# Performance work log

Measured on AMD Instinct MI355X. Metric: run time of the kernel, lower is better.

The kernel has to match this reference:

```python
import jax, jax.numpy as jnp
import numpy as np

EPS = 1.1920929e-07  # torch RMSNorm default eps = finfo(fp32).eps


def _rmsnorm(x, w):
    return x * jax.lax.rsqrt(jnp.mean(x * x, axis=-1, keepdims=True) + EPS) * w


def setup_inputs() -> dict:
    B, S, D, H, SD = 2, 2048, 1024, 16, 64
    ks = jax.random.split(jax.random.key(0), 16)
    scale = 0.02
    return {
        "x": jax.random.normal(ks[0], (B, S, D), jnp.float32),
        "gamma": jax.random.normal(ks[1], (1, 1, D), jnp.float32),
        "beta": jax.random.normal(ks[2], (1, 1, D), jnp.float32),
        "state": jax.random.normal(ks[3], (B, SD), jnp.float32),
        # weights stored as (in, out) so y = x @ W
        "w_qkv": jax.random.normal(ks[4], (D, 3 * D), jnp.float32) * scale,
        "w_o": jax.random.normal(ks[5], (D, D), jnp.float32) * scale,
        "w_gate": jax.random.normal(ks[6], (D, 3 * D), jnp.float32) * scale,
        "w_up": jax.random.normal(ks[7], (D, 3 * D), jnp.float32) * scale,
        "w_down": jax.random.normal(ks[8], (3 * D, D), jnp.float32) * scale,
        "norm1_w": jnp.ones((D,), jnp.float32),
        "norm2_w": jnp.ones((D,), jnp.float32),
        "w_state_mod": jax.random.normal(ks[9], (SD, 2 * D), jnp.float32) * scale,
        "w_h2s": jax.random.normal(ks[10], (D, SD), jnp.float32) * scale,
        "w_sgate": jax.random.normal(ks[11], (2 * SD, SD), jnp.float32) * scale,
    }


def reference(x, gamma, beta, state, w_qkv, w_o, w_gate, w_up, w_down,
              norm1_w, norm2_w, w_state_mod, w_h2s, w_sgate):
    B, S, D = x.shape
    H = 16
    hd = D // H

    # state-conditioned FiLM modulation
    state_mod = state @ w_state_mod                      # (B, 2D)
    state_gamma = 1.0 + state_mod[:, :D][:, None, :]     # (B, 1, D)
    state_beta = state_mod[:, D:][:, None, :]
    full_gamma = gamma * state_gamma
    full_beta = beta + state_beta

    # attention branch
    h = _rmsnorm(x, norm1_w) * full_gamma + full_beta
    qkv = (h @ w_qkv).reshape(B, S, 3, H, hd)
    q = qkv[:, :, 0].transpose(0, 2, 1, 3)               # (B, H, S, hd)
    k = qkv[:, :, 1].transpose(0, 2, 1, 3)
    v = qkv[:, :, 2].transpose(0, 2, 1, 3)
    scores = jnp.einsum('bhqd,bhkd->bhqk', q, k) / np.sqrt(hd).astype(np.float32)
    causal = jnp.tril(jnp.ones((S, S), bool))
    scores = jnp.where(causal, scores, -jnp.inf)
    attn = jax.nn.softmax(scores, axis=-1)
    out = jnp.einsum('bhqk,bhkd->bhqd', attn, v).transpose(0, 2, 1, 3).reshape(B, S, D)
    x = x + out @ w_o

    # SwiGLU FFN branch (same FiLM params)
    h2 = _rmsnorm(x, norm2_w) * full_gamma + full_beta
    gate = jax.nn.silu(h2 @ w_gate)
    x = x + (gate * (h2 @ w_up)) @ w_down

    # recurrent state update
    new_info = jnp.mean(x, axis=1) @ w_h2s               # (B, SD)
    update_gate = jax.nn.sigmoid(jnp.concatenate([state, new_info], axis=-1) @ w_sgate)
    new_state = state * (1.0 - update_gate) + new_info * update_gate
    return x, new_state
```

## Files before the change

kernel.cpp:

```cpp
#include <hip/hip_runtime.h>
#include <hip/hip_bf16.h>

#define EPS_RMS 1.1920929e-07f

constexpr int B_ = 2, S_ = 2048, D_ = 1024, H_ = 16, HD_ = 64, SD_ = 64;
constexpr int M_ = B_ * S_;
constexpr int D3_ = 3 * D_;

using short8 = __attribute__((ext_vector_type(8))) short;
using f32x4  = __attribute__((ext_vector_type(4))) float;
using f32x16 = __attribute__((ext_vector_type(16))) float;
typedef int v2i __attribute__((ext_vector_type(2)));

static __device__ __forceinline__ ushort f2bf(float x) {
  __hip_bfloat16 h = __float2bfloat16(x);
  return *reinterpret_cast<ushort*>(&h);
}
static __device__ __forceinline__ float bf2f(ushort u) {
  __hip_bfloat16 h;
  *reinterpret_cast<ushort*>(&h) = u;
  return __bfloat162float(h);
}
static __device__ __forceinline__ unsigned pk2(float lo, float hi) {
  return (unsigned)f2bf(lo) | ((unsigned)f2bf(hi) << 16);
}
static __device__ __forceinline__ v2i swap32(int a, int b) {
  return __builtin_amdgcn_permlane32_swap(a, b, false, false);
}
struct alignas(8) bf4 { ushort a, b, c, d; };

static __device__ __forceinline__ void gload16(const ushort* g, ushort* l) {
  __builtin_amdgcn_global_load_lds(
      (const __attribute__((address_space(1))) unsigned int*)g,
      (__attribute__((address_space(3))) unsigned int*)l, 16, 0, 0);
}

__global__ void film_kernel(const float* __restrict__ state,
                            const float* __restrict__ w_sm,
                            const float* __restrict__ gamma,
                            const float* __restrict__ beta,
                            float* __restrict__ fg, float* __restrict__ fb) {
  int c = blockIdx.x * 256 + threadIdx.x;
  int b = blockIdx.y;
  float acc = 0.f;
#pragma unroll 8
  for (int k = 0; k < SD_; ++k)
    acc += state[b * SD_ + k] * w_sm[k * (2 * D_) + c];
  if (c < D_) fg[b * D_ + c] = gamma[c] * (1.f + acc);
  else        fb[b * D_ + (c - D_)] = beta[c - D_] + acc;
}

__global__ __launch_bounds__(256) void rmsnorm_film_kernel(
    const float* __restrict__ X, const float* __restrict__ nw,
    const float* __restrict__ fg, const float* __restrict__ fb,
    ushort* __restrict__ Hout) {
  int row = blockIdx.x;
  int b = row / S_;
  int t = threadIdx.x;
  const float4* x4 = (const float4*)(X + (size_t)row * D_);
  float4 xv = x4[t];
  float ss = xv.x * xv.x + xv.y * xv.y + xv.z * xv.z + xv.w * xv.w;
#pragma unroll
  for (int off = 32; off >= 1; off >>= 1) ss += __shfl_xor(ss, off);
  __shared__ float red[4];
  if ((t & 63) == 0) red[t >> 6] = ss;
  __syncthreads();
  float tot = red[0] + red[1] + red[2] + red[3];
  float scale = rsqrtf(tot / (float)D_ + EPS_RMS);
  int d = t * 4;
  const float4 nw4 = *(const float4*)(nw + d);
  const float4 g4  = *(const float4*)(fg + b * D_ + d);
  const float4 b4  = *(const float4*)(fb + b * D_ + d);
  bf4 hv;
  hv.a = f2bf(xv.x * scale * nw4.x * g4.x + b4.x);
  hv.b = f2bf(xv.y * scale * nw4.y * g4.y + b4.y);
  hv.c = f2bf(xv.z * scale * nw4.z * g4.z + b4.z);
  hv.d = f2bf(xv.w * scale * nw4.w * g4.w + b4.w);
  *(bf4*)(Hout + (size_t)row * D_ + d) = hv;
}

__global__ __launch_bounds__(256) void transpose_bf16(
    const float* __restrict__ W, ushort* __restrict__ Wt, int K, int N) {
  __shared__ float tile[32][33];
  int n0 = blockIdx.x * 32, k0 = blockIdx.y * 32;
  int t = threadIdx.x;
  int c = t & 31, r = t >> 5;
#pragma unroll
  for (int p = 0; p < 4; ++p)
    tile[r + 8 * p][c] = W[(size_t)(k0 + r + 8 * p) * N + n0 + c];
  __syncthreads();
#pragma unroll
  for (int p = 0; p < 4; ++p)
    Wt[(size_t)(n0 + r + 8 * p) * K + k0 + c] = f2bf(tile[c][r + 8 * p]);
}

__global__ __launch_bounds__(256) void transpose_bf16_dual(
    const float* __restrict__ W0, ushort* __restrict__ T0,
    const float* __restrict__ W1, ushort* __restrict__ T1, int K, int N) {
  const float* W = blockIdx.z ? W1 : W0;
  ushort* Wt = blockIdx.z ? T1 : T0;
  __shared__ float tile[32][33];
  int n0 = blockIdx.x * 32, k0 = blockIdx.y * 32;
  int t = threadIdx.x;
  int c = t & 31, r = t >> 5;
#pragma unroll
  for (int p = 0; p < 4; ++p)
    tile[r + 8 * p][c] = W[(size_t)(k0 + r + 8 * p) * N + n0 + c];
  __syncthreads();
#pragma unroll
  for (int p = 0; p < 4; ++p)
    Wt[(size_t)(n0 + r + 8 * p) * K + k0 + c] = f2bf(tile[c][r + 8 * p]);
}

static __device__ __forceinline__ void mfma_tile(
    const char* Au, const char* Bu, f32x4 (&acc)[4][4],
    int l15, int l4, int swz, int wr, int wc) {
#pragma unroll
  for (int kk = 0; kk < 2; ++kk) {
    int tslot = ((kk * 4 + l4) ^ swz) << 4;
    short8 a[4], b[4];
#pragma unroll
    for (int i = 0; i < 4; ++i) {
      int arow = wr * 64 + i * 16 + l15;
      int brow = wc * 64 + i * 16 + l15;
      a[i] = *(const short8*)(Au + arow * 128 + tslot);
      b[i] = *(const short8*)(Bu + brow * 128 + tslot);
    }
#pragma unroll
    for (int m = 0; m < 4; ++m)
#pragma unroll
      for (int n = 0; n < 4; ++n)
        acc[m][n] = __builtin_amdgcn_mfma_f32_16x16x32_bf16(a[m], b[n], acc[m][n], 0, 0, 0);
  }
}

static __device__ __forceinline__ void block_swizzle(int bid, int M, int N,
                                                     int& bm, int& bn) {
  int nbn = N >> 7;
  int nb  = nbn * (M >> 7);
  int qx  = nb >> 3;
  int lin = (bid & 7) * qx + (bid >> 3);
  int grp = lin / (nbn << 3), rem = lin % (nbn << 3);
  bm = ((grp << 3) + (rem & 7)) << 7;
  bn = (rem >> 3) << 7;
}

template<int EPI>
__global__ __launch_bounds__(256, 3) void gemm_mfma(
    const ushort* __restrict__ A, const ushort* __restrict__ Bt,
    const float* __restrict__ Res,
    float* __restrict__ Cf, ushort* __restrict__ Cb, ushort* __restrict__ VtP,
    int M, int N, int K) {
  __shared__ ushort smem[16384];
  char* Au = (char*)smem;
  char* Bu = (char*)(smem + 8192);
  int t = threadIdx.x;
  int bm, bn;
  block_swizzle(blockIdx.x, M, N, bm, bn);

  int lane = t & 63, wid = t >> 6;
  int wr = wid >> 1, wc = wid & 1;
  int l15 = lane & 15, l4 = lane >> 4;
  int swz = l15 & 7;

  const ushort* gA[4];
  const ushort* gB[4];
  ushort* lA[4];
  ushort* lB[4];
#pragma unroll
  for (int p = 0; p < 4; ++p) {
    int seg = p * 4 + wid;
    int flat = seg * 64 + lane;
    int row = flat >> 3, sl = flat & 7;
    int gc = ((sl ^ (row & 7)) << 3);
    gA[p] = A  + (size_t)(bm + row) * K + gc;
    gB[p] = Bt + (size_t)(bn + row) * K + gc;
    lA[p] = smem + seg * 512;
    lB[p] = smem + 8192 + seg * 512;
  }

  f32x4 acc[4][4];
#pragma unroll
  for (int m = 0; m < 4; ++m)
#pragma unroll
    for (int n = 0; n < 4; ++n) acc[m][n] = (f32x4){0.f, 0.f, 0.f, 0.f};

  int nk = K >> 6;
  for (int kt = 0; kt < nk; ++kt) {
    __syncthreads();
#pragma unroll
    for (int p = 0; p < 4; ++p) {
      gload16(gA[p], lA[p]);
      gload16(gB[p], lB[p]);
      gA[p] += 64; gB[p] += 64;
    }
    __syncthreads();
    mfma_tile(Au, Bu, acc, l15, l4, swz, wr, wc);
  }

  if constexpr (EPI == 3) {
#pragma unroll
    for (int m = 0; m < 4; ++m)
#pragma unroll
      for (int n = 0; n < 4; ++n) {
        int row0 = bm + wr * 64 + m * 16 + l4 * 4;
        int col  = bn + wc * 64 + n * 16 + l15;
#pragma unroll
        for (int j = 0; j < 4; ++j) {
          size_t idx = (size_t)(row0 + j) * (size_t)N + col;
          Cf[idx] = Res[idx] + acc[m][n][j];
        }
      }
  } else {
    __syncthreads();
    ushort* Es = smem;
    bool vblk = (bn >= 2048);
#pragma unroll
    for (int m = 0; m < 4; ++m)
#pragma unroll
      for (int n = 0; n < 4; ++n) {
        int rb0 = wr * 64 + m * 16 + l4 * 4;
        int c   = wc * 64 + n * 16 + l15;
#pragma unroll
        for (int j = 0; j < 4; ++j) {
          float v = acc[m][n][j];
          int r = rb0 + j;
          if (vblk) Es[c * 128 + (r ^ ((c & 15) << 3))] = f2bf(v);
          else      Es[r * 128 + c] = f2bf(v);
        }
      }
    __syncthreads();
    if (vblk) {
#pragma unroll
      for (int p = 0; p < 8; ++p) {
        int flat = p * 256 + t;
        int c = flat >> 4, r8 = (flat & 15) * 8;
        int vc = bn - 2048 + c, hh = vc >> 6, dd = vc & 63;
        int bbv = bm >> 11, s0 = (bm & 2047) + r8;
        *(short8*)(VtP + ((((size_t)bbv * 16 + hh) * 64 + dd) << 11) + s0) =
            *(const short8*)&Es[c * 128 + (r8 ^ ((c & 15) << 3))];
      }
    } else {
#pragma unroll
      for (int p = 0; p < 8; ++p) {
        int flat = p * 256 + t;
        int r = flat >> 4, c8 = (flat & 15) * 8;
        *(short8*)(Cb + (size_t)(bm + r) * N + bn + c8) = *(const short8*)&Es[r * 128 + c8];
      }
    }
  }
}

__global__ __launch_bounds__(256, 2) void gemm_dual(
    const ushort* __restrict__ A, const ushort* __restrict__ Gt,
    const ushort* __restrict__ Ut, ushort* __restrict__ Cb,
    int M, int N, int K) {
  __shared__ ushort smem[24576];
  char* Au = (char*)smem;
  char* Gu = (char*)(smem + 8192);
  char* Uu = (char*)(smem + 16384);
  int t = threadIdx.x;
  int bm, bn;
  block_swizzle(blockIdx.x, M, N, bm, bn);

  int lane = t & 63, wid = t >> 6;
  int wr = wid >> 1, wc = wid & 1;
  int l15 = lane & 15, l4 = lane >> 4;
  int swz = l15 & 7;

  const ushort* gA[4]; const ushort* gG[4]; const ushort* gU[4];
  ushort* lA[4]; ushort* lG[4]; ushort* lU[4];
#pragma unroll
  for (int p = 0; p < 4; ++p) {
    int seg = p * 4 + wid;
    int flat = seg * 64 + lane;
    int row = flat >> 3, sl = flat & 7;
    int gc = ((sl ^ (row & 7)) << 3);
    gA[p] = A  + (size_t)(bm + row) * K + gc;
    gG[p] = Gt + (size_t)(bn + row) * K + gc;
    gU[p] = Ut + (size_t)(bn + row) * K + gc;
    lA[p] = smem + seg * 512;
    lG[p] = smem + 8192 + seg * 512;
    lU[p] = smem + 16384 + seg * 512;
  }

  f32x4 ag[4][4], au[4][4];
#pragma unroll
  for (int m = 0; m < 4; ++m)
#pragma unroll
    for (int n = 0; n < 4; ++n) {
      ag[m][n] = (f32x4){0.f, 0.f, 0.f, 0.f};
      au[m][n] = (f32x4){0.f, 0.f, 0.f, 0.f};
    }

  int nk = K >> 6;
  for (int kt = 0; kt < nk; ++kt) {
    __syncthreads();
#pragma unroll
    for (int p = 0; p < 4; ++p) {
      gload16(gA[p], lA[p]);
      gload16(gG[p], lG[p]);
      gload16(gU[p], lU[p]);
      gA[p] += 64; gG[p] += 64; gU[p] += 64;
    }
    __syncthreads();
#pragma unroll
    for (int kk = 0; kk < 2; ++kk) {
      int tslot = ((kk * 4 + l4) ^ swz) << 4;
      short8 a[4], bg[4], bu[4];
#pragma unroll
      for (int i = 0; i < 4; ++i) {
        int arow = wr * 64 + i * 16 + l15;
        int brow = wc * 64 + i * 16 + l15;
        a[i]  = *(const short8*)(Au + arow * 128 + tslot);
        bg[i] = *(const short8*)(Gu + brow * 128 + tslot);
        bu[i] = *(const short8*)(Uu + brow * 128 + tslot);
      }
#pragma unroll
      for (int m = 0; m < 4; ++m)
#pragma unroll
        for (int n = 0; n < 4; ++n) {
          ag[m][n] = __builtin_amdgcn_mfma_f32_16x16x32_bf16(a[m], bg[n], ag[m][n], 0, 0, 0);
          au[m][n] = __builtin_amdgcn_mfma_f32_16x16x32_bf16(a[m], bu[n], au[m][n], 0, 0, 0);
        }
    }
  }

  __syncthreads();
  ushort* Es = smem;
#pragma unroll
  for (int m = 0; m < 4; ++m)
#pragma unroll
    for (int n = 0; n < 4; ++n) {
      int rb0 = wr * 64 + m * 16 + l4 * 4;
      int c   = wc * 64 + n * 16 + l15;
#pragma unroll
      for (int j = 0; j < 4; ++j) {
        float gv = ag[m][n][j];
        float v = gv / (1.f + __expf(-gv)) * au[m][n][j];
        Es[(rb0 + j) * 128 + c] = f2bf(v);
      }
    }
  __syncthreads();
#pragma unroll
  for (int p = 0; p < 8; ++p) {
    int flat = p * 256 + t;
    int r = flat >> 4, c8 = (flat & 15) * 8;
    *(short8*)(Cb + (size_t)(bm + r) * N + bn + c8) = *(const short8*)&Es[r * 128 + c8];
  }
}

__global__ __launch_bounds__(512, 2) void attn_mfma_kernel(
    const ushort* __restrict__ qkv,
    const ushort* __restrict__ Vt,
    ushort* __restrict__ AO) {
  __shared__ ushort lds[16384];
  const float SL2 = 0.125f * 1.44269504f;
  int t = threadIdx.x;
  int x = blockIdx.x;
  int lin = ((x & 7) << 5) + (x >> 3);
  int pp = lin & 7;
  int hb = lin >> 3;
  int h = hb & 15, bb = hb >> 4;
  int lane = t & 63, wv = t >> 6;
  int qi = wv >> 2, wsub = wv & 3;
  int qt = qi ? (15 - pp) : pp;
  int q0 = qt * 128;
  int l31 = lane & 31, g = lane >> 5;

  int qrow = q0 + wsub * 32 + l31;
  const ushort* qrow_ptr = qkv + (size_t)(bb * S_ + qrow) * 3072 + h * 64;
  short8 qf[4];
#pragma unroll
  for (int s = 0; s < 4; ++s) qf[s] = *(const short8*)(qrow_ptr + s * 16 + g * 8);

  f32x16 accO[2];
#pragma unroll
  for (int u = 0; u < 2; ++u)
#pragma unroll
    for (int r = 0; r < 16; ++r) accO[u][r] = 0.f;
  float m = -INFINITY, l = 0.f;
  int qg = qrow;
  int qmin = q0 + wsub * 32, qmax = qmin + 31;
  int nt = 2 * (16 - pp);

  const ushort* kbase = qkv + (size_t)(bb * S_) * 3072 + 1024 + h * 64;
  const ushort* vbase = Vt + ((size_t)(bb * 16 + h) * 64) * 2048;

  int srow = t >> 3, sslot = t & 7;
  int soff = srow * 64 + ((sslot ^ (srow & 7)) << 3);
  const ushort* kg0 = kbase + (size_t)srow * 3072 + sslot * 8;
  const ushort* vg0 = vbase + (size_t)srow * 2048 + sslot * 8;

  *(short8*)&lds[soff] = *(const short8*)kg0;
  *(short8*)&lds[4096 + soff] = *(const short8*)vg0;
  __syncthreads();

  for (int kti = 0; kti < nt; ++kti) {
    int cur = kti & 1;
    int kt = kti << 6;
    bool pf = (kti + 1 < nt);
    short8 rk, rv;
    if (pf) {
      rk = *(const short8*)(kg0 + (size_t)(kti + 1) * (64 * 3072));
      rv = *(const short8*)(vg0 + (kti + 1) * 64);
    }
    if (kt <= qmax) {
      const ushort* Kb = lds + cur * 8192;
      const ushort* Vb = Kb + 4096;

      f32x16 accT[2];
#pragma unroll
      for (int t2 = 0; t2 < 2; ++t2)
#pragma unroll
        for (int r = 0; r < 16; ++r) accT[t2][r] = 0.f;
      __builtin_amdgcn_s_setprio(1);
#pragma unroll
      for (int t2 = 0; t2 < 2; ++t2) {
        int key = 32 * t2 + l31;
#pragma unroll
        for (int s = 0; s < 4; ++s) {
          short8 kf = *(const short8*)&Kb[key * 64 + (((2 * s + g) ^ (key & 7)) << 3)];
          accT[t2] = __builtin_amdgcn_mfma_f32_32x32x16_bf16(kf, qf[s], accT[t2], 0, 0, 0);
        }
      }
      __builtin_amdgcn_s_setprio(0);

      bool need_mask = (kt + 63 > qmin);
      float p_[2][16];
      float pmax = -INFINITY;
#pragma unroll
      for (int t2 = 0; t2 < 2; ++t2)
#pragma unroll
        for (int r = 0; r < 16; ++r) {
          float v = accT[t2][r] * SL2;
          if (need_mask) {
            int key = kt + 32 * t2 + (r & 3) + 8 * (r >> 2) + 4 * g;
            if (key > qg) v = -INFINITY;
          }
          p_[t2][r] = v;
          pmax = fmaxf(pmax, v);
        }
      {
        v2i pm = swap32(__float_as_int(pmax), __float_as_int(pmax));
        pmax = fmaxf(pmax, __int_as_float(g ? pm.x : pm.y));
      }

      if (__any(pmax > m + 11.5f)) {
        float mnew = fmaxf(m, pmax);
        float corr = exp2f(m - mnew);
        m = mnew;
        l *= corr;
        float cr[16];
#pragma unroll
        for (int r = 0; r < 16; ++r) cr[r] = __shfl(corr, (r & 3) + 8 * (r >> 2) + 4 * g);
#pragma unroll
        for (int r = 0; r < 16; ++r) { accO[0][r] *= cr[r]; accO[1][r] *= cr[r]; }
      }
      float psum = 0.f;
#pragma unroll
      for (int t2 = 0; t2 < 2; ++t2)
#pragma unroll
        for (int r = 0; r < 16; ++r) {
          float e = exp2f(p_[t2][r] - m);
          p_[t2][r] = e;
          psum += e;
        }
      {
        v2i ps = swap32(__float_as_int(psum), __float_as_int(psum));
        psum += __int_as_float(g ? ps.x : ps.y);
      }
      l += psum;

#pragma unroll
      for (int s = 0; s < 4; ++s) {
        int ca = 2 * s, cb2 = 2 * s + 1;
        int ta = ca >> 2, ra = (ca & 3) * 4;
        int tb = cb2 >> 2, rbq = (cb2 & 3) * 4;
        int w0a = (int)pk2(p_[ta][ra], p_[ta][ra + 1]);
        int w1a = (int)pk2(p_[ta][ra + 2], p_[ta][ra + 3]);
        int w0b = (int)pk2(p_[tb][rbq], p_[tb][rbq + 1]);
        int w1b = (int)pk2(p_[tb][rbq + 2], p_[tb][rbq + 3]);
        v2i r0 = swap32(w0a, w0b);
        v2i r1 = swap32(w1a, w1b);
        union { int u[4]; short8 s8; } pa;
        pa.u[0] = r0.x;
        pa.u[1] = r1.x;
        pa.u[2] = r0.y;
        pa.u[3] = r1.y;
        __builtin_amdgcn_s_setprio(1);
#pragma unroll
        for (int u = 0; u < 2; ++u) {
          int d = 32 * u + l31;
          short8 vf = *(const short8*)&Vb[d * 64 + (((2 * s + g) ^ (d & 7)) << 3)];
          accO[u] = __builtin_amdgcn_mfma_f32_32x32x16_bf16(pa.s8, vf, accO[u], 0, 0, 0);
        }
        __builtin_amdgcn_s_setprio(0);
      }
    }
    if (pf) {
      ushort* dst = lds + (cur ^ 1) * 8192;
      *(short8*)&dst[soff] = rk;
      *(short8*)&dst[4096 + soff] = rv;
    }
    __syncthreads();
  }

  float linv = 1.f / l;
  float lr[16];
#pragma unroll
  for (int r = 0; r < 16; ++r) lr[r] = __shfl(linv, (r & 3) + 8 * (r >> 2) + 4 * g);
#pragma unroll
  for (int r = 0; r < 16; ++r) {
    int row = wv * 32 + (r & 3) + 8 * (r >> 2) + 4 * g;
    lds[row * 64 + l31]      = f2bf(accO[0][r] * lr[r]);
    lds[row * 64 + 32 + l31] = f2bf(accO[1][r] * lr[r]);
  }
  __syncthreads();
#pragma unroll
  for (int p = 0; p < 4; ++p) {
    int flat = p * 512 + t;
    int row = flat >> 3, slot = flat & 7;
    int qto = (row < 128) ? pp : (15 - pp);
    int grow = row & 127;
    *(short8*)(AO + (size_t)(bb * S_ + qto * 128 + grow) * 1024 + h * 64 + slot * 8) =
        *(const short8*)&lds[row * 64 + slot * 8];
  }
}

__global__ void colmean1(const float* __restrict__ X, float* __restrict__ part) {
  int d = blockIdx.x * 256 + threadIdx.x;
  int b = blockIdx.y;
  int ch = blockIdx.z;
  float s = 0.f;
  int s0 = ch * (S_ / 16);
  for (int i = 0; i < S_ / 16; ++i)
    s += X[(size_t)(b * S_ + s0 + i) * D_ + d];
  part[(b * 16 + ch) * D_ + d] = s;
}

__global__ __launch_bounds__(1024) void colmean2_state_kernel(
    const float* __restrict__ part, const float* __restrict__ state,
    const float* __restrict__ w_h2s, const float* __restrict__ w_sg,
    float* __restrict__ out_tail) {
  __shared__ float cms[2048];
  __shared__ float nis[128];
  int t = threadIdx.x;
#pragma unroll
  for (int i = 0; i < 2; ++i) {
    int idx = i * 1024 + t;
    int b = idx >> 10, d = idx & 1023;
    float s = 0.f;
#pragma unroll
    for (int c = 0; c < 16; ++c) s += part[(b * 16 + c) * D_ + d];
    cms[idx] = s * (1.f / (float)S_);
  }
  __syncthreads();
  {
    int out = t >> 3, ks = t & 7;
    int b = out >> 6, j = out & 63;
    float ni = 0.f;
    int k0 = ks * 128;
#pragma unroll 8
    for (int k = k0; k < k0 + 128; ++k)
      ni += cms[b * 1024 + k] * w_h2s[k * SD_ + j];
    ni += __shfl_xor(ni, 1);
    ni += __shfl_xor(ni, 2);
    ni += __shfl_xor(ni, 4);
    if (ks == 0) nis[out] = ni;
  }
  __syncthreads();
  if (t < 128) {
    int b = t >> 6, j = t & 63;
    float nv = nis[t];
    float g = 0.f;
#pragma unroll
    for (int k = 0; k < SD_; ++k) g += state[b * SD_ + k] * w_sg[k * SD_ + j];
#pragma unroll
    for (int k = 0; k < SD_; ++k) g += nis[b * SD_ + k] * w_sg[(SD_ + k) * SD_ + j];
    g = 1.f / (1.f + __expf(-g));
    float st = state[b * SD_ + j];
    out_tail[t] = st * (1.f - g) + nv * g;
  }
}

extern "C" void kernel_launch(void* const* d_in, const int* in_sizes, int n_in,
                              void* d_out, int out_size, void* d_ws, size_t ws_size,
                              hipStream_t stream) {
  const float* x      = (const float*)d_in[0];
  const float* gamma  = (const float*)d_in[1];
  const float* beta   = (const float*)d_in[2];
  const float* state  = (const float*)d_in[3];
  const float* w_qkv  = (const float*)d_in[4];
  const float* w_o    = (const float*)d_in[5];
  const float* w_gate = (const float*)d_in[6];
  const float* w_up   = (const float*)d_in[7];
  const float* w_down = (const float*)d_in[8];
  const float* norm1w = (const float*)d_in[9];
  const float* norm2w = (const float*)d_in[10];
  const float* w_sm   = (const float*)d_in[11];
  const float* w_h2s  = (const float*)d_in[12];
  const float* w_sg   = (const float*)d_in[13];
  float* out = (float*)d_out;

  float* ws = (float*)d_ws;
  float*  fg     = ws;
  float*  fb     = ws + 2048;
  float*  part   = ws + 8192;
  ushort* h_bf   = (ushort*)(ws + 65536);
  ushort* AO_bf  = (ushort*)(ws + 65536 + 2097152);
  ushort* wT     = (ushort*)(ws + 65536 + 2 * 2097152);
  ushort* wT2    = (ushort*)(ws + 65536 + 2 * 2097152 + 1572864);
  ushort* qkv_bf = (ushort*)(ws + 65536 + 2 * 2097152 + 2 * 1572864);
  ushort* Vt_g   = (ushort*)(ws + 65536 + 2 * 2097152 + 2 * 1572864 + 6291456);
  ushort* gu_bf  = qkv_bf;

  film_kernel<<<dim3(8, B_), 256, 0, stream>>>(state, w_sm, gamma, beta, fg, fb);
  rmsnorm_film_kernel<<<M_, 256, 0, stream>>>(x, norm1w, fg, fb, h_bf);
  transpose_bf16<<<dim3(D3_ / 32, D_ / 32), 256, 0, stream>>>(w_qkv, wT, D_, D3_);
  gemm_mfma<4><<<(D3_ / 128) * (M_ / 128), 256, 0, stream>>>(
      h_bf, wT, nullptr, nullptr, qkv_bf, Vt_g, M_, D3_, D_);
  attn_mfma_kernel<<<256, 512, 0, stream>>>(qkv_bf, Vt_g, AO_bf);
  transpose_bf16<<<dim3(D_ / 32, D_ / 32), 256, 0, stream>>>(w_o, wT, D_, D_);
  gemm_mfma<3><<<(D_ / 128) * (M_ / 128), 256, 0, stream>>>(
      AO_bf, wT, x, out, nullptr, nullptr, M_, D_, D_);
  rmsnorm_film_kernel<<<M_, 256, 0, stream>>>(out, norm2w, fg, fb, h_bf);
  transpose_bf16_dual<<<dim3(D3_ / 32, D_ / 32, 2), 256, 0, stream>>>(
      w_gate, wT, w_up, wT2, D_, D3_);
  gemm_dual<<<(D3_ / 128) * (M_ / 128), 256, 0, stream>>>(
      h_bf, wT, wT2, gu_bf, M_, D3_, D_);
  transpose_bf16<<<dim3(D_ / 32, D3_ / 32), 256, 0, stream>>>(w_down, wT, D3_, D_);
  gemm_mfma<3><<<(D_ / 128) * (M_ / 128), 256, 0, stream>>>(
      gu_bf, wT, out, out, nullptr, nullptr, M_, D_, D3_);
  colmean1<<<dim3(4, B_, 16), 256, 0, stream>>>(out, part);
  colmean2_state_kernel<<<1, 1024, 0, stream>>>(part, state, w_h2s, w_sg,
                                                out + (size_t)M_ * D_);
}
```

Measured before the change: 308.6 us.

## Split attention key range across two blocks and merge partials in a separate kernel

The causal attention kernel now launches twice as many blocks. Each block processes every other 64-key tile (even or odd) and writes unnormalized bf16 partial outputs plus running max and sum. A new merge kernel combines the two partials with log-sum-exp rescaling and writes the final attention output. The aim is more parallelism and occupancy on the GPU. The cost is an extra kernel launch, partial-output traffic through global memory, bf16 rounding of the unnormalized partials, and raised launch-bounds occupancy targets that may cause register spills.

New measurement: 296.1 us (median of 2 runs). -4.0%, faster.

```diff
diff --git a/kernel.cpp b/kernel.cpp
--- a/kernel.cpp
+++ b/kernel.cpp
@@ -6,6 +6,7 @@
 constexpr int B_ = 2, S_ = 2048, D_ = 1024, H_ = 16, HD_ = 64, SD_ = 64;
 constexpr int M_ = B_ * S_;
 constexpr int D3_ = 3 * D_;
+constexpr int NT2_ = 512 * 512;
 
 using short8 = __attribute__((ext_vector_type(8))) short;
 using f32x4  = __attribute__((ext_vector_type(4))) float;
@@ -146,7 +147,7 @@
 }
 
 template<int EPI>
-__global__ __launch_bounds__(256, 3) void gemm_mfma(
+__global__ __launch_bounds__(256, 4) void gemm_mfma(
     const ushort* __restrict__ A, const ushort* __restrict__ Bt,
     const float* __restrict__ Res,
     float* __restrict__ Cf, ushort* __restrict__ Cb, ushort* __restrict__ VtP,
@@ -350,17 +351,19 @@
   }
 }
 
-__global__ __launch_bounds__(512, 2) void attn_mfma_kernel(
+__global__ __launch_bounds__(512, 4) void attn_mfma_kernel(
     const ushort* __restrict__ qkv,
     const ushort* __restrict__ Vt,
-    ushort* __restrict__ AO) {
+    unsigned* __restrict__ PO,
+    float* __restrict__ PM, float* __restrict__ PL) {
   __shared__ ushort lds[16384];
   const float SL2 = 0.125f * 1.44269504f;
   int t = threadIdx.x;
   int x = blockIdx.x;
-  int lin = ((x & 7) << 5) + (x >> 3);
-  int pp = lin & 7;
-  int hb = lin >> 3;
+  int lin = ((x & 7) << 6) + (x >> 3);
+  int kh = lin & 1;
+  int pp = (lin >> 1) & 7;
+  int hb = lin >> 4;
   int h = hb & 15, bb = hb >> 4;
   int lane = t & 63, wv = t >> 6;
   int qi = wv >> 2, wsub = wv & 3;
@@ -382,7 +385,8 @@
   float m = -INFINITY, l = 0.f;
   int qg = qrow;
   int qmin = q0 + wsub * 32, qmax = qmin + 31;
-  int nt = 2 * (16 - pp);
+  int ntpair = 2 * (16 - pp);
+  int ntk = (ntpair - kh + 1) >> 1;
 
   const ushort* kbase = qkv + (size_t)(bb * S_) * 3072 + 1024 + h * 64;
   const ushort* vbase = Vt + ((size_t)(bb * 16 + h) * 64) * 2048;
@@ -392,18 +396,19 @@
   const ushort* kg0 = kbase + (size_t)srow * 3072 + sslot * 8;
   const ushort* vg0 = vbase + (size_t)srow * 2048 + sslot * 8;
 
-  *(short8*)&lds[soff] = *(const short8*)kg0;
-  *(short8*)&lds[4096 + soff] = *(const short8*)vg0;
-  __syncthreads();
-
-  for (int kti = 0; kti < nt; ++kti) {
-    int cur = kti & 1;
+  *(short8*)&lds[soff] = *(const short8*)(kg0 + (size_t)kh * (64 * 3072));
+  *(short8*)&lds[4096 + soff] = *(const short8*)(vg0 + kh * 64);
+  __syncthreads();
+
+  for (int i2 = 0; i2 < ntk; ++i2) {
+    int cur = i2 & 1;
+    int kti = 2 * i2 + kh;
     int kt = kti << 6;
-    bool pf = (kti + 1 < nt);
+    bool pf = (i2 + 1 < ntk);
     short8 rk, rv;
     if (pf) {
-      rk = *(const short8*)(kg0 + (size_t)(kti + 1) * (64 * 3072));
-      rv = *(const short8*)(vg0 + (kti + 1) * 64);
+      rk = *(const short8*)(kg0 + (size_t)(kti + 2) * (64 * 3072));
+      rv = *(const short8*)(vg0 + (kti + 2) * 64);
     }
     if (kt <= qmax) {
       const ushort* Kb = lds + cur * 8192;
@@ -506,15 +511,52 @@
     __syncthreads();
   }
 
-  float linv = 1.f / l;
-  float lr[16];
-#pragma unroll
-  for (int r = 0; r < 16; ++r) lr[r] = __shfl(linv, (r & 3) + 8 * (r >> 2) + 4 * g);
+  size_t base = (size_t)lin * 512 + t;
+#pragma unroll
+  for (int r = 0; r < 16; ++r)
+    PO[(size_t)r * NT2_ + base] = pk2(accO[0][r], accO[1][r]);
+  PM[base] = m;
+  PL[base] = l;
+}
+
+__global__ __launch_bounds__(512, 2) void attn_merge_kernel(
+    const unsigned* __restrict__ PO, const float* __restrict__ PM,
+    const float* __restrict__ PL, ushort* __restrict__ AO) {
+  __shared__ ushort lds[16384];
+  int t = threadIdx.x;
+  int xb = blockIdx.x;
+  int lin2 = ((xb & 7) << 5) + (xb >> 3);
+  int pp = lin2 & 7;
+  int hb = lin2 >> 3;
+  int h = hb & 15, bb = hb >> 4;
+  int lane = t & 63, wv = t >> 6;
+  int l31 = lane & 31, g = lane >> 5;
+
+  size_t p0 = ((size_t)((hb << 4) | (pp << 1)) * 512) + t;
+  size_t p1 = p0 + 512;
+  float m0 = PM[p0], l0 = PL[p0];
+  float m1 = PM[p1], l1 = PL[p1];
+  float mn = fmaxf(m0, m1);
+  float c0 = exp2f(m0 - mn), c1 = exp2f(m1 - mn);
+  float linv = 1.f / (l0 * c0 + l1 * c1);
+
+  float cr0[16], cr1[16], lr[16];
 #pragma unroll
   for (int r = 0; r < 16; ++r) {
+    int src = (r & 3) + 8 * (r >> 2) + 4 * g;
+    cr0[r] = __shfl(c0, src);
+    cr1[r] = __shfl(c1, src);
+    lr[r]  = __shfl(linv, src);
+  }
+#pragma unroll
+  for (int r = 0; r < 16; ++r) {
+    unsigned u0 = PO[(size_t)r * NT2_ + p0];
+    unsigned u1 = PO[(size_t)r * NT2_ + p1];
+    float a0 = bf2f((ushort)(u0 & 0xffff)), b0 = bf2f((ushort)(u0 >> 16));
+    float a1 = bf2f((ushort)(u1 & 0xffff)), b1 = bf2f((ushort)(u1 >> 16));
     int row = wv * 32 + (r & 3) + 8 * (r >> 2) + 4 * g;
-    lds[row * 64 + l31]      = f2bf(accO[0][r] * lr[r]);
-    lds[row * 64 + 32 + l31] = f2bf(accO[1][r] * lr[r]);
+    lds[row * 64 + l31]      = f2bf((a0 * cr0[r] + a1 * cr1[r]) * lr[r]);
+    lds[row * 64 + 32 + l31] = f2bf((b0 * cr0[r] + b1 * cr1[r]) * lr[r]);
   }
   __syncthreads();
 #pragma unroll
@@ -608,11 +650,14 @@
   float*  fb     = ws + 2048;
   float*  part   = ws + 8192;
   ushort* h_bf   = (ushort*)(ws + 65536);
-  ushort* AO_bf  = (ushort*)(ws + 65536 + 2097152);
-  ushort* wT     = (ushort*)(ws + 65536 + 2 * 2097152);
-  ushort* wT2    = (ushort*)(ws + 65536 + 2 * 2097152 + 1572864);
-  ushort* qkv_bf = (ushort*)(ws + 65536 + 2 * 2097152 + 2 * 1572864);
-  ushort* Vt_g   = (ushort*)(ws + 65536 + 2 * 2097152 + 2 * 1572864 + 6291456);
+  ushort* wT     = (ushort*)(ws + 65536 + 2097152);
+  ushort* wT2    = (ushort*)(ws + 65536 + 3670016);
+  unsigned* PO   = (unsigned*)(ws + 65536);
+  float*  PM     = ws + 65536 + 4194304;
+  float*  PL     = ws + 65536 + 4456448;
+  ushort* AO_bf  = (ushort*)(ws + 65536 + 5242880);
+  ushort* qkv_bf = (ushort*)(ws + 65536 + 7340032);
+  ushort* Vt_g   = (ushort*)(ws + 65536 + 13631488);
   ushort* gu_bf  = qkv_bf;
 
   film_kernel<<<dim3(8, B_), 256, 0, stream>>>(state, w_sm, gamma, beta, fg, fb);
@@ -620,7 +665,8 @@
   transpose_bf16<<<dim3(D3_ / 32, D_ / 32), 256, 0, stream>>>(w_qkv, wT, D_, D3_);
   gemm_mfma<4><<<(D3_ / 128) * (M_ / 128), 256, 0, stream>>>(
       h_bf, wT, nullptr, nullptr, qkv_bf, Vt_g, M_, D3_, D_);
-  attn_mfma_kernel<<<256, 512, 0, stream>>>(qkv_bf, Vt_g, AO_bf);
+  attn_mfma_kernel<<<512, 512, 0, stream>>>(qkv_bf, Vt_g, PO, PM, PL);
+  attn_merge_kernel<<<256, 512, 0, stream>>>(PO, PM, PL, AO_bf);
   transpose_bf16<<<dim3(D_ / 32, D_ / 32), 256, 0, stream>>>(w_o, wT, D_, D_);
   gemm_mfma<3><<<(D_ / 128) * (M_ / 128), 256, 0, stream>>>(
       AO_bf, wT, x, out, nullptr, nullptr, M_, D_, D_);
```
